# Kernel optimization log

Measured on AMD Instinct MI355X. Metric: run time of the kernel, lower is better.

## Reference

```python
import jax, jax.numpy as jnp
import numpy as np
from math import comb

G, NPG, D = 32, 128, 128   # graphs, nodes-per-graph, hidden dim
N = G * NPG                # 4096 nodes per side
E = 65536                  # edges per side (avg degree 16)
K = 6                      # Bernstein order (bern_k)
S, DCONV, DTR = 16, 4, 8   # mamba d_state, d_conv, dt_rank
HE = 27
SIGMAS = [1.0, 10.0, 100.0, 1000.0, 10000.0]


def _leaky(x, s=0.02):
    return jnp.where(x >= 0, x, s * x)


def _bnorm(x, g, b, eps=1e-5):
    m = jnp.mean(x, axis=0)
    v = jnp.var(x, axis=0)
    return (x - m) * jax.lax.rsqrt(v + eps) * g + b


def _bern_prop(x, src, dst, w, temp):
    # BernNet Bern_prop: Bernstein polynomial of sym-normalized Laplacian with weights relu(temp)
    n = x.shape[0]
    temp = jax.nn.relu(temp)
    deg = jax.ops.segment_sum(w, src, num_segments=n)
    dinv = jnp.where(deg > 0, 1.0 / jnp.sqrt(deg + 1e-12), 0.0)
    nw = (w * dinv[src] * dinv[dst])[:, None]
    adj = lambda v: jax.ops.segment_sum(nw * v[src], dst, num_segments=n)
    tmps = [x]
    xv = x
    for _ in range(K):
        xv = xv + adj(xv)          # (2I - L) v = v + A_norm v
        tmps.append(xv)
    out = (comb(K, 0) / 2 ** K) * temp[0] * tmps[K]
    for i in range(K):
        v = tmps[K - i - 1]
        for _ in range(i + 1):
            v = v - adj(v)         # L v = v - A_norm v
        out = out + (comb(K, i + 1) / 2 ** K) * temp[i + 1] * v
    return out


def _mamba(h, in_w, conv_w, conv_b, xproj_w, dt_w, dt_b, A_log, Dp, out_w):
    # Mamba block, d_model=D, expand=1 (d_inner=D), d_state=S, d_conv=DCONV
    Bb, L, _ = h.shape
    xq, z = jnp.split(h @ in_w, 2, axis=-1)             # [B,L,D] each
    xp = jnp.pad(xq, ((0, 0), (DCONV - 1, 0), (0, 0)))  # causal depthwise conv
    xc = conv_b + sum(xp[:, k:k + L, :] * conv_w[:, k] for k in range(DCONV))
    xc = jax.nn.silu(xc)
    dbl = xc @ xproj_w                                  # [B,L,DTR+2S]
    dt = jax.nn.softplus(dbl[..., :DTR] @ dt_w + dt_b)  # [B,L,D]
    Bm = dbl[..., DTR:DTR + S]
    Cm = dbl[..., DTR + S:]
    A = -jnp.exp(A_log)                                 # [D,S]
    dA = jnp.exp(dt[..., None] * A)                     # [B,L,D,S]
    dBx = dt[..., None] * Bm[:, :, None, :] * xc[..., None]

    def step(hs, ins):
        dA_t, dBx_t, C_t = ins
        hs = dA_t * hs + dBx_t
        return hs, jnp.einsum('bds,bs->bd', hs, C_t)

    h0 = jnp.zeros((Bb, D, S), h.dtype)
    _, ys = jax.lax.scan(step, h0, (jnp.swapaxes(dA, 0, 1),
                                    jnp.swapaxes(dBx, 0, 1),
                                    jnp.swapaxes(Cm, 0, 1)))
    y = jnp.swapaxes(ys, 0, 1) + xc * Dp
    return (y * jax.nn.silu(z)) @ out_w


def _xattn(q, k, v, mask):
    a = mask * (q @ k.T) - 1000.0 * (1.0 - mask)
    return jax.nn.softmax(a, axis=1) @ v


def setup_inputs():
    key = jax.random.key(0)
    ks = jax.random.split(key, 32)
    f = jnp.float32
    nrm = lambda k, shp, sc=1.0: jax.random.normal(k, shp, dtype=f) * sc
    h_lig = nrm(ks[0], (N, D), 0.5)
    h_rec = nrm(ks[1], (N, D), 0.5)
    x_lig = nrm(ks[2], (N, 3))
    x_rec = nrm(ks[3], (N, 3))
    he_1 = jax.random.uniform(ks[4], (E, HE), dtype=f)
    he_2 = jax.random.uniform(ks[5], (E, HE), dtype=f)
    g = (jnp.arange(E) // (E // G)).astype(jnp.int32)
    src1 = g * NPG + jax.random.randint(ks[6], (E,), 0, NPG, dtype=jnp.int32)
    dst1 = g * NPG + jax.random.randint(ks[7], (E,), 0, NPG, dtype=jnp.int32)
    src2 = g * NPG + jax.random.randint(ks[8], (E,), 0, NPG, dtype=jnp.int32)
    dst2 = g * NPG + jax.random.randint(ks[9], (E,), 0, NPG, dtype=jnp.int32)
    edge_index_1 = jnp.stack([src1, dst1])
    edge_index_2 = jnp.stack([src2, dst2])
    batch = (jnp.arange(N) // NPG).astype(jnp.int32)
    rng = np.random.default_rng(0)
    def mkperm(src):
        # lexsort([deg + noise, batch]) with batch as primary key
        deg = np.bincount(np.asarray(src), minlength=N).astype(np.float32)
        return jnp.asarray(np.lexsort((deg + rng.random(N).astype(np.float32),
                                       np.asarray(batch))).astype(np.int32))
    perm_1 = mkperm(src1)
    perm_2 = mkperm(src2)
    p = {}
    p['emlp_w1'] = nrm(ks[10], (32, D), 0.1)
    p['emlp_b1'] = jnp.zeros((D,), f)
    p['emlp_bn_g'] = jnp.ones((D,), f)
    p['emlp_bn_b'] = jnp.zeros((D,), f)
    p['emlp_w2'] = nrm(ks[11], (D, 1), 0.1)
    p['emlp_b2'] = jnp.zeros((1,), f)
    p['bern_temp'] = jnp.ones((K + 1,), f)
    p['m_in_w'] = nrm(ks[12], (D, 2 * D), 0.05)
    p['m_conv_w'] = nrm(ks[13], (D, DCONV), 0.2)
    p['m_conv_b'] = jnp.zeros((D,), f)
    p['m_xproj_w'] = nrm(ks[14], (D, DTR + 2 * S), 0.05)
    p['m_dt_w'] = nrm(ks[15], (DTR, D), 0.2)
    p['m_dt_b'] = jnp.full((D,), -4.0, f)
    p['m_A_log'] = jnp.log(jnp.broadcast_to(jnp.arange(1, S + 1, dtype=f), (D, S)))
    p['m_D'] = jnp.ones((D,), f)
    p['m_out_w'] = nrm(ks[16], (D, D), 0.05)
    p['q_w'] = nrm(ks[17], (D, D), 0.05)
    p['k_w'] = nrm(ks[18], (D, D), 0.05)
    p['v_w'] = nrm(ks[19], (D, D), 0.05)
    p['bn1_g'] = jnp.ones((D,), f)
    p['bn1_b'] = jnp.zeros((D,), f)
    p['bn2_g'] = jnp.ones((D,), f)
    p['bn2_b'] = jnp.zeros((D,), f)
    p['ff_w1'] = nrm(ks[20], (D, 2 * D), 0.05)
    p['ff_b1'] = jnp.zeros((2 * D,), f)
    p['ff_w2'] = nrm(ks[21], (2 * D, D), 0.05)
    p['ff_b2'] = jnp.zeros((D,), f)
    return dict(h_lig=h_lig, h_rec=h_rec, x_lig=x_lig, x_rec=x_rec,
                he_1=he_1, he_2=he_2, **p,
                edge_index_1=edge_index_1, edge_index_2=edge_index_2,
                batch_1=batch, batch_2=batch, perm_1=perm_1, perm_2=perm_2)


def reference(h_lig, h_rec, x_lig, x_rec, he_1, he_2,
              emlp_w1, emlp_b1, emlp_bn_g, emlp_bn_b, emlp_w2, emlp_b2,
              bern_temp, m_in_w, m_conv_w, m_conv_b, m_xproj_w, m_dt_w,
              m_dt_b, m_A_log, m_D, m_out_w, q_w, k_w, v_w,
              bn1_g, bn1_b, bn2_g, bn2_b, ff_w1, ff_b1, ff_w2, ff_b2,
              edge_index_1, edge_index_2, batch_1, batch_2, perm_1, perm_2):

    def side(h, x, he, ei, perm):
        src, dst = ei[0], ei[1]
        d2 = jnp.sum((x[src] - x[dst]) ** 2, axis=1, keepdims=True)
        ew = jnp.concatenate([jnp.exp(-d2 / s) for s in SIGMAS], axis=1)  # [E,5]
        t = _leaky(jnp.concatenate([ew, he], axis=1) @ emlp_w1 + emlp_b1)
        t = _bnorm(t, emlp_bn_g, emlp_bn_b)
        w = jax.nn.relu(t @ emlp_w2 + emlp_b2)[:, 0]                      # [E]
        h_local = _bern_prop(h, src, dst, w, bern_temp)
        inv = jnp.argsort(perm)
        hd = h[perm].reshape(G, NPG, D)   # uniform graph sizes -> exact dense batch
        ha = _mamba(hd, m_in_w, m_conv_w, m_conv_b, m_xproj_w, m_dt_w,
                    m_dt_b, m_A_log, m_D, m_out_w).reshape(N, D)[inv]
        return _bnorm(h + h_local + ha, bn1_g, bn1_b)

    hl = side(h_lig, x_lig, he_1, edge_index_1, perm_1)
    hr = side(h_rec, x_rec, he_2, edge_index_2, perm_2)
    mask = (batch_1[:, None] == batch_2[None, :]).astype(hl.dtype)
    cl = _xattn(_leaky(hl @ q_w), _leaky(hr @ k_w), hr @ v_w, mask)
    cr = _xattn(_leaky(hr @ q_w), _leaky(hl @ k_w), hl @ v_w, mask.T)
    hl = hl + cl
    hr = hr + cr
    ff = lambda h: jax.nn.relu(h @ ff_w1 + ff_b1) @ ff_w2 + ff_b2
    hl = _bnorm(hl + ff(hl), bn2_g, bn2_b)
    hr = _bnorm(hr + ff(hr), bn2_g, bn2_b)
    return hl, hr
```

## Files before the change

### kernel.cpp

```cpp
#include <hip/hip_runtime.h>
#include <math.h>

#define G_    32
#define NPG_  128
#define D_    128
#define N_    4096
#define E_    65536
#define ND_   (N_*D_)

#define W_OFF     0
#define DEG_OFF   65536
#define STATS_OFF 69632
#define BUF0      71680
#define HL_OFF    (BUF0 + 0*ND_)
#define HA_OFF    (BUF0 + 1*ND_)
#define X1_OFF    (BUF0 + 2*ND_)
#define HMID_OFF  (BUF0 + 3*ND_)
#define XC_OFF    (BUF0 + 4*ND_)
#define DTB_OFF   (BUF0 + 5*ND_)
#define YB_OFF    (BUF0 + 6*ND_)
#define XZ_OFF    (BUF0 + 7*ND_)
#define DBL_OFF   (BUF0 + 9*ND_)
#define SS_       ((size_t)(DBL_OFF + N_*40))

__device__ __forceinline__ float leakyf(float x){ return x >= 0.f ? x : 0.02f*x; }
__device__ __forceinline__ float siluf (float x){ return x / (1.f + expf(-x)); }

__device__ __forceinline__ void edge_feat(const float* __restrict__ x,
                                          const float* __restrict__ he,
                                          const int* __restrict__ ei,
                                          int e, float* feat, int& sN, int& dN)
{
  sN = ei[e]; dN = ei[E_ + e];
  float dx = x[sN*3+0]-x[dN*3+0];
  float dy = x[sN*3+1]-x[dN*3+1];
  float dz = x[sN*3+2]-x[dN*3+2];
  float d2 = dx*dx + dy*dy + dz*dz;
  feat[0] = expf(-d2/1.f);
  feat[1] = expf(-d2/10.f);
  feat[2] = expf(-d2/100.f);
  feat[3] = expf(-d2/1000.f);
  feat[4] = expf(-d2/10000.f);
#pragma unroll
  for (int j = 0; j < 27; ++j) feat[5+j] = he[(size_t)e*27 + j];
}

__global__ __launch_bounds__(256)
void edge_stats_kernel(const float* __restrict__ xl, const float* __restrict__ xr,
                       const float* __restrict__ hel, const float* __restrict__ her,
                       const int* __restrict__ ei1, const int* __restrict__ ei2,
                       const float* __restrict__ w1, const float* __restrict__ b1,
                       float* __restrict__ ws)
{
  int side = blockIdx.y;
  const float* x  = side ? xr  : xl;
  const float* he = side ? her : hel;
  const int*   ei = side ? ei2 : ei1;
  float* stats = ws + (size_t)side*SS_ + STATS_OFF;
  __shared__ float featl[256*36];
  __shared__ float csum[2][128], cssq[2][128];
  int tid = threadIdx.x;
  {
    int sN, dN; float feat[32];
    edge_feat(x, he, ei, blockIdx.x*256 + tid, feat, sN, dN);
#pragma unroll
    for (int j4 = 0; j4 < 8; ++j4)
      *(float4*)&featl[tid*36 + j4*4] = *(float4*)&feat[j4*4];
  }
  int c = tid & 127, hh = tid >> 7;
  float w1c[32];
#pragma unroll
  for (int j = 0; j < 32; ++j) w1c[j] = w1[j*128 + c];
  float b1c = b1[c];
  __syncthreads();
  float s1 = 0.f, s2 = 0.f;
  for (int e = 0; e < 128; ++e) {
    const float* f = &featl[(hh*128 + e)*36];
    float acc = b1c;
#pragma unroll
    for (int j4 = 0; j4 < 8; ++j4) {
      float4 f4 = *(const float4*)&f[j4*4];
      acc += f4.x*w1c[j4*4] + f4.y*w1c[j4*4+1] + f4.z*w1c[j4*4+2] + f4.w*w1c[j4*4+3];
    }
    float t = leakyf(acc);
    s1 += t; s2 += t*t;
  }
  csum[hh][c] = s1; cssq[hh][c] = s2;
  __syncthreads();
  if (tid < 128) {
    atomicAdd(&stats[tid],     csum[0][tid] + csum[1][tid]);
    atomicAdd(&stats[128+tid], cssq[0][tid] + cssq[1][tid]);
  }
}

__global__ void edge_finalize_kernel(const float* __restrict__ g_, const float* __restrict__ b_,
                                     const float* __restrict__ w2, const float* __restrict__ b2,
                                     float* __restrict__ ws)
{
  int side = blockIdx.y;
  float* stats = ws + (size_t)side*SS_ + STATS_OFF;
  __shared__ float red[128];
  int c = threadIdx.x;
  const float invE = 1.f/(float)E_;
  float mean = stats[c]*invE;
  float var  = fmaxf(stats[128+c]*invE - mean*mean, 0.f);
  float scale = rsqrtf(var + 1e-5f) * g_[c];
  stats[256+c] = scale * w2[c];
  red[c] = (b_[c] - mean*scale) * w2[c];
  __syncthreads();
  for (int off = 64; off; off >>= 1) { if (c < off) red[c] += red[c+off]; __syncthreads(); }
  if (c == 0) stats[384] = red[0] + b2[0];
}

__global__ __launch_bounds__(256)
void edge_w_kernel(const float* __restrict__ xl, const float* __restrict__ xr,
                   const float* __restrict__ hel, const float* __restrict__ her,
                   const int* __restrict__ ei1, const int* __restrict__ ei2,
                   const float* __restrict__ w1, const float* __restrict__ b1,
                   float* __restrict__ ws)
{
  int side = blockIdx.y;
  const float* x  = side ? xr  : xl;
  const float* he = side ? her : hel;
  const int*   ei = side ? ei2 : ei1;
  float* base = ws + (size_t)side*SS_;
  const float* stats = base + STATS_OFF;
  float* wbuf = base + W_OFF;
  float* deg  = base + DEG_OFF;
  __shared__ float w1t[128*32];
  __shared__ float b1l[128], all_[128];
  int tid = threadIdx.x;
  for (int i = tid; i < 4096; i += 256) {
    int j = i & 31, c = i >> 5;
    w1t[c*32 + j] = w1[j*128 + c];
  }
  if (tid < 128) { b1l[tid] = b1[tid]; all_[tid] = stats[256+tid]; }
  __syncthreads();
  int e = blockIdx.x*256 + tid;
  int sN, dN; float feat[32];
  edge_feat(x, he, ei, e, feat, sN, dN);
  float accw = stats[384];
  for (int c = 0; c < 128; ++c) {
    float acc = b1l[c];
#pragma unroll
    for (int j4 = 0; j4 < 8; ++j4) {
      float4 w4 = *(const float4*)&w1t[c*32 + j4*4];
      acc += feat[j4*4]*w4.x + feat[j4*4+1]*w4.y + feat[j4*4+2]*w4.z + feat[j4*4+3]*w4.w;
    }
    accw += leakyf(acc)*all_[c];
  }
  float w = fmaxf(accw, 0.f);
  wbuf[e] = w;
  atomicAdd(&deg[sN], w);
}

__global__ __launch_bounds__(256)
void bern_horner_kernel(const float* __restrict__ hl_in, const float* __restrict__ hr_in,
                        const int* __restrict__ ei1, const int* __restrict__ ei2,
                        const float* __restrict__ bern_temp, float* __restrict__ ws)
{
  int side = blockIdx.y;
  int g  = blockIdx.x >> 2;
  int d0 = (blockIdx.x & 3) * 32;
  const float* h  = side ? hr_in : hl_in;
  const int*   ei = side ? ei2 : ei1;
  float* base = ws + (size_t)side*SS_;
  const float* wbuf = base + W_OFF;
  const float* deg  = base + DEG_OFF;
  float* hloc = base + HL_OFF;

  __shared__ float A[128*132];
  __shared__ float v[128*32];
  int tid = threadIdx.x;
  for (int i = tid; i < 128*132; i += 256) A[i] = 0.f;

  const float btab[7][7] = {
    { 1,  6, 15,  20, 15,  6,  1},
    { 1,  4,  5,   0, -5, -4, -1},
    { 1,  2, -1,  -4, -1,  2,  1},
    { 1,  0, -3,   0,  3,  0, -1},
    { 1, -2, -1,   4, -1, -2,  1},
    { 1, -4,  5,   0, -5,  4, -1},
    { 1, -6, 15, -20, 15, -6,  1}};
  const float comb6[7] = {1,6,15,20,15,6,1};
  float a[7];
#pragma unroll
  for (int m = 0; m < 7; ++m) a[m] = 0.f;
#pragma unroll
  for (int j = 0; j < 7; ++j) {
    float tj = fmaxf(bern_temp[j], 0.f) * comb6[j] * (1.f/64.f);
#pragma unroll
    for (int m = 0; m < 7; ++m) a[m] += tj * btab[j][m];
  }
  __syncthreads();

  int ebase = g*2048, nbase = g*128;
  for (int i = tid; i < 2048; i += 256) {
    int e = ebase + i;
    int sN = ei[e], dN = ei[E_ + e];
    float ds_ = deg[sN], dd_ = deg[dN];
    float aa = ds_ > 0.f ? rsqrtf(ds_ + 1e-12f) : 0.f;
    float bb = dd_ > 0.f ? rsqrtf(dd_ + 1e-12f) : 0.f;
    atomicAdd(&A[(dN - nbase)*132 + (sN - nbase)], wbuf[e]*aa*bb);
  }

  const int db = (tid & 7)*4;
  const int rb = (tid >> 3)*4;
  float hreg[4][4], r[4][4], t[4][4];
#pragma unroll
  for (int i = 0; i < 4; ++i) {
    float4 h4 = *(const float4*)&h[(size_t)(nbase + rb + i)*128 + d0 + db];
    hreg[i][0]=h4.x; hreg[i][1]=h4.y; hreg[i][2]=h4.z; hreg[i][3]=h4.w;
#pragma unroll
    for (int jj = 0; jj < 4; ++jj) r[i][jj] = a[6]*hreg[i][jj];
  }

  for (int step = 5; step >= 0; --step) {
    __syncthreads();
#pragma unroll
    for (int i = 0; i < 4; ++i)
      *(float4*)&v[(rb+i)*32 + db] = make_float4(r[i][0], r[i][1], r[i][2], r[i][3]);
    __syncthreads();
#pragma unroll
    for (int i = 0; i < 4; ++i)
#pragma unroll
      for (int jj = 0; jj < 4; ++jj) t[i][jj] = 0.f;
    for (int k = 0; k < 128; k += 4) {
      float4 V0 = *(const float4*)&v[(k+0)*32 + db];
      float4 V1 = *(const float4*)&v[(k+1)*32 + db];
      float4 V2 = *(const float4*)&v[(k+2)*32 + db];
      float4 V3 = *(const float4*)&v[(k+3)*32 + db];
#pragma unroll
      for (int i = 0; i < 4; ++i) {
        float4 A4 = *(const float4*)&A[(rb+i)*132 + k];
        t[i][0] += A4.x*V0.x + A4.y*V1.x + A4.z*V2.x + A4.w*V3.x;
        t[i][1] += A4.x*V0.y + A4.y*V1.y + A4.z*V2.y + A4.w*V3.y;
        t[i][2] += A4.x*V0.z + A4.y*V1.z + A4.z*V2.z + A4.w*V3.z;
        t[i][3] += A4.x*V0.w + A4.y*V1.w + A4.z*V2.w + A4.w*V3.w;
      }
    }
    float ak = a[step];
#pragma unroll
    for (int i = 0; i < 4; ++i)
#pragma unroll
      for (int jj = 0; jj < 4; ++jj) r[i][jj] = t[i][jj] + ak*hreg[i][jj];
  }

#pragma unroll
  for (int i = 0; i < 4; ++i)
    *(float4*)&hloc[(size_t)(nbase + rb + i)*128 + d0 + db] =
        make_float4(r[i][0], r[i][1], r[i][2], r[i][3]);
}

template<int K, int NC, int TC, int CSPLIT, int ACT, int GATHER, int SCATTER, int ADDC, int BIAS>
__global__ __launch_bounds__(256)
void gemm_kernel(const float* __restrict__ A0, const float* __restrict__ A1, int lda,
                 const float* __restrict__ W, const float* __restrict__ bias,
                 float* __restrict__ C0, float* __restrict__ C1, int ldc,
                 const int* __restrict__ idx0, const int* __restrict__ idx1,
                 const float* __restrict__ add0, const float* __restrict__ add1)
{
  int side = blockIdx.y;
  const float* A = side ? A1 : A0;
  float* C = side ? C1 : C0;
  const int* idx = side ? idx1 : idx0;
  const float* addsrc = side ? add1 : add0;
  constexpr int RPT = TC/8;
  constexpr int CLEN = NC/CSPLIT;
  __shared__ float Alds[32][K];
  __shared__ float Wlds[K][TC];
  const int tid = threadIdx.x;
  const int r0 = (blockIdx.x / CSPLIT) * 32;
  const int cbase = (blockIdx.x % CSPLIT) * CLEN;
  for (int i = tid*4; i < 32*K; i += 1024) {
    int r = i / K, k = i % K;
    int row = GATHER ? idx[r0 + r] : (r0 + r);
    *(float4*)&Alds[r][k] = *(const float4*)&A[(size_t)row*lda + k];
  }
  for (int c0 = cbase; c0 < cbase + CLEN; c0 += TC) {
    __syncthreads();
    for (int i = tid*4; i < K*TC; i += 1024) {
      int k = i / TC, c = i % TC;
      if (c0 + c < NC) *(float4*)&Wlds[k][c] = *(const float4*)&W[k*NC + c0 + c];
      else             *(float4*)&Wlds[k][c] = make_float4(0.f,0.f,0.f,0.f);
    }
    __syncthreads();
    const int cl = tid % TC;
    const int rsub = (tid / TC) * RPT;
    float accv[RPT];
#pragma unroll
    for (int j = 0; j < RPT; ++j) accv[j] = 0.f;
    for (int k = 0; k < K; k += 4) {
      float w0 = Wlds[k][cl], w1v = Wlds[k+1][cl], w2v = Wlds[k+2][cl], w3v = Wlds[k+3][cl];
#pragma unroll
      for (int j = 0; j < RPT; ++j) {
        float4 a4 = *(const float4*)&Alds[rsub+j][k];
        accv[j] += a4.x*w0 + a4.y*w1v + a4.z*w2v + a4.w*w3v;
      }
    }
    int c = c0 + cl;
    if (c < NC) {
#pragma unroll
      for (int j = 0; j < RPT; ++j) {
        int row  = r0 + rsub + j;
        int orow = SCATTER ? idx[row] : row;
        float vv = accv[j];
        if (BIAS)     vv += bias[c];
        if (ACT == 1) vv = leakyf(vv);
        if (ACT == 2) vv = fmaxf(vv, 0.f);
        if (ADDC)     vv += addsrc[(size_t)orow*ldc + c];
        C[(size_t)orow*ldc + c] = vv;
      }
    }
  }
}

__global__ __launch_bounds__(256)
void qkv_kernel(const float* __restrict__ qw, const float* __restrict__ kw,
                const float* __restrict__ vw, float* __restrict__ ws)
{
  int side = blockIdx.y;
  int mat  = blockIdx.z;
  float* base = ws + (size_t)side*SS_;
  const float* A = base + HMID_OFF;
  const float* W = mat == 0 ? qw : (mat == 1 ? kw : vw);
  float* C = base + (mat == 0 ? XC_OFF : (mat == 1 ? DTB_OFF : YB_OFF));
  __shared__ float Alds[32][128];
  __shared__ float Wlds[128][64];
  const int tid = threadIdx.x;
  const int r0 = (blockIdx.x >> 1) * 32;
  const int c0 = (blockIdx.x & 1) * 64;
  for (int i = tid*4; i < 32*128; i += 1024)
    *(float4*)&Alds[i>>7][i&127] = *(const float4*)&A[(size_t)(r0 + (i>>7))*128 + (i&127)];
  for (int i = tid*4; i < 128*64; i += 1024)
    *(float4*)&Wlds[i>>6][i&63] = *(const float4*)&W[(i>>6)*128 + c0 + (i&63)];
  __syncthreads();
  const int cl = tid & 63;
  const int rsub = (tid >> 6) * 8;
  float accv[8];
#pragma unroll
  for (int j = 0; j < 8; ++j) accv[j] = 0.f;
  for (int k = 0; k < 128; k += 4) {
    float w0 = Wlds[k][cl], w1v = Wlds[k+1][cl], w2v = Wlds[k+2][cl], w3v = Wlds[k+3][cl];
#pragma unroll
    for (int j = 0; j < 8; ++j) {
      float4 a4 = *(const float4*)&Alds[rsub+j][k];
      accv[j] += a4.x*w0 + a4.y*w1v + a4.z*w2v + a4.w*w3v;
    }
  }
#pragma unroll
  for (int j = 0; j < 8; ++j) {
    float vv = accv[j];
    if (mat < 2) vv = leakyf(vv);
    C[(size_t)(r0 + rsub + j)*128 + c0 + cl] = vv;
  }
}

__global__ __launch_bounds__(256)
void conv_kernel(const float* __restrict__ cw, const float* __restrict__ cb, float* __restrict__ ws)
{
  int side = blockIdx.y;
  float* base = ws + (size_t)side*SS_;
  const float* xz = base + XZ_OFF;
  float* xc = base + XC_OFF;
  int i = blockIdx.x*256 + threadIdx.x;
  int j = i >> 7, d = i & 127;
  int l = j & 127;
  float a = cb[d];
#pragma unroll
  for (int k = 0; k < 4; ++k) {
    int ll = l - 3 + k;
    if (ll >= 0) a += xz[(size_t)(j-3+k)*256 + d] * cw[d*4 + k];
  }
  xc[i] = siluf(a);
}

__global__ __launch_bounds__(256)
void scan_kernel(const float* __restrict__ A_log, const float* __restrict__ Dp,
                 const float* __restrict__ dtw, const float* __restrict__ dtbias,
                 float* __restrict__ ws)
{
  int side = blockIdx.z;
  int g  = blockIdx.x;
  int d0 = blockIdx.y * 16;
  float* base = ws + (size_t)side*SS_;
  const float* dbl = base + DBL_OFF;
  const float* xcb = base + XC_OFF;
  float* xz = base + XZ_OFF;

  __shared__ float ldbl[128][40];
  __shared__ float lxc[128][16];
  __shared__ float ldt[128][16];
  __shared__ float lz[128][16];
  __shared__ float ly[128][16];
  __shared__ float ltw[8][16];
  __shared__ float ltb[16];

  int tid = threadIdx.x;
  int rowbase = g*128;
  if (tid < 128)      ltw[tid>>4][tid&15] = dtw[(tid>>4)*128 + d0 + (tid&15)];
  else if (tid < 144) ltb[tid-128] = dtbias[d0 + (tid-128)];
  for (int i = tid; i < 128*40; i += 256)
    ((float*)ldbl)[i] = dbl[(size_t)rowbase*40 + i];
  for (int i = tid; i < 2048; i += 256) {
    int l = i >> 4, dd = i & 15;
    lxc[l][dd] = xcb[(size_t)(rowbase+l)*128 + d0 + dd];
    lz[l][dd]  = xz[(size_t)(rowbase+l)*256 + 128 + d0 + dd];
  }
  __syncthreads();
  for (int i = tid; i < 2048; i += 256) {
    int l = i >> 4, dd = i & 15;
    float a = ltb[dd];
#pragma unroll
    for (int k = 0; k < 8; ++k) a += ldbl[l][k]*ltw[k][dd];
    ldt[l][dd] = a > 20.f ? a : log1pf(expf(a));
  }
  __syncthreads();

  int s = tid & 15, dl = (tid >> 4) & 15;
  float Ac  = -expf(A_log[(d0+dl)*16 + s]);
  float dpv = Dp[d0+dl];
  float hsv = 0.f;
  for (int l = 0; l < 128; ++l) {
    float dtv = ldt[l][dl];
    float xcv = lxc[l][dl];
    float Bv  = ldbl[l][8+s];
    float Cv  = ldbl[l][24+s];
    hsv = expf(dtv*Ac)*hsv + (dtv*xcv)*Bv;
    float val = hsv*Cv;
    val += __shfl_xor(val, 1, 16);
    val += __shfl_xor(val, 2, 16);
    val += __shfl_xor(val, 4, 16);
    val += __shfl_xor(val, 8, 16);
    if (s == 0) ly[l][dl] = val + xcv*dpv;
  }
  __syncthreads();
  for (int i = tid; i < 2048; i += 256) {
    int l = i >> 4, dd = i & 15;
    float y = ly[l][dd];
    float z = lz[l][dd];
    xz[(size_t)(rowbase+l)*256 + d0 + dd] = y * siluf(z);
  }
}

__global__ __launch_bounds__(256)
void stats_kernel(const float* __restrict__ hl_in, const float* __restrict__ hr_in,
                  float* __restrict__ ws, int mode, int statsoff)
{
  int side = blockIdx.y;
  float* base = ws + (size_t)side*SS_;
  const float* h    = side ? hr_in : hl_in;
  const float* hloc = base + HL_OFF;
  const float* ha   = base + HA_OFF;
  float* x1 = base + X1_OFF;
  float* stats = base + STATS_OFF + statsoff;
  int tid = threadIdx.x;
  int c = tid & 127;
  float s1 = 0.f, s2 = 0.f;
  for (int it = 0; it < 16; ++it) {
    int r = blockIdx.x*32 + (tid >> 7) + it*2;
    size_t i = (size_t)r*128 + c;
    float v;
    if (mode == 0) { v = h[i] + hloc[i] + ha[i]; x1[i] = v; }
    else           { v = ha[i]; }
    s1 += v; s2 += v*v;
  }
  __shared__ float red[256];
  red[tid] = s1; __syncthreads();
  if (tid < 128) atomicAdd(&stats[tid], red[tid] + red[tid+128]);
  __syncthreads();
  red[tid] = s2; __syncthreads();
  if (tid < 128) atomicAdd(&stats[128+tid], red[tid] + red[tid+128]);
}

__global__ void bn_finalize_kernel(const float* __restrict__ g_, const float* __restrict__ b_,
                                   float* __restrict__ ws, int statsoff, float invM)
{
  int side = blockIdx.y;
  float* stats = ws + (size_t)side*SS_ + STATS_OFF + statsoff;
  int c = threadIdx.x;
  float mean = stats[c]*invM;
  float var  = fmaxf(stats[128+c]*invM - mean*mean, 0.f);
  float scale = rsqrtf(var + 1e-5f) * g_[c];
  stats[256+c] = scale;
  stats[384+c] = b_[c] - mean*scale;
}

__global__ __launch_bounds__(256)
void bn_apply_kernel(float* __restrict__ ws, float* __restrict__ dout,
                     int srcoff, int dstoff, int statsoff, int to_dout)
{
  int side = blockIdx.y;
  float* base = ws + (size_t)side*SS_;
  const float* src = base + srcoff;
  const float* stats = base + STATS_OFF + statsoff;
  float* dst = to_dout ? (dout + (size_t)side*ND_) : (base + dstoff);
  size_t i = (size_t)blockIdx.x*256 + threadIdx.x;
  int c = (int)(i & 127);
  dst[i] = src[i]*stats[256+c] + stats[384+c];
}

__global__ __launch_bounds__(256)
void attn_kernel(float* __restrict__ ws)
{
  int dir = blockIdx.z;
  int g   = blockIdx.x;
  int rt  = blockIdx.y;
  float* baseq = ws + (size_t)dir*SS_;
  float* basek = ws + (size_t)(1-dir)*SS_;
  const float* qb = baseq + XC_OFF;
  const float* kb = basek + DTB_OFF;
  const float* vb = basek + YB_OFF;
  const float* hm = baseq + HMID_OFF;
  float* h2 = baseq + X1_OFF;
  __shared__ float kT[128*129];
  __shared__ float sp[32*128];
  int tid = threadIdx.x;
  for (int i = tid; i < 16384; i += 256) {
    int n = i >> 7, d = i & 127;
    kT[d*129 + n] = kb[(size_t)(g*128+n)*128 + d];
  }
  __syncthreads();
  int wv = tid >> 6, lane = tid & 63;
  for (int rl = wv; rl < 32; rl += 4) {
    int r = g*128 + rt*32 + rl;
    const float* qrow = qb + (size_t)r*128;
    float a0 = 0.f, a1 = 0.f;
    for (int d = 0; d < 128; ++d) {
      float qv = qrow[d];
      a0 += qv * kT[d*129 + lane];
      a1 += qv * kT[d*129 + 64 + lane];
    }
    float m = fmaxf(a0, a1);
#pragma unroll
    for (int off = 32; off; off >>= 1) m = fmaxf(m, __shfl_xor(m, off));
    float p0 = expf(a0 - m), p1 = expf(a1 - m);
    float ssum = p0 + p1;
#pragma unroll
    for (int off = 32; off; off >>= 1) ssum += __shfl_xor(ssum, off);
    float inv = 1.f/ssum;
    sp[rl*128 + lane]      = p0*inv;
    sp[rl*128 + 64 + lane] = p1*inv;
  }
  __syncthreads();
  for (int i = tid; i < 16384; i += 256) {
    int n = i >> 7, d = i & 127;
    kT[n*129 + d] = vb[(size_t)(g*128+n)*128 + d];
  }
  __syncthreads();
  for (int rl = wv; rl < 32; rl += 4) {
    int r = g*128 + rt*32 + rl;
    float a0 = 0.f, a1 = 0.f;
    const float* prow = sp + rl*128;
    for (int c = 0; c < 128; ++c) {
      float p = prow[c];
      a0 += p * kT[c*129 + lane];
      a1 += p * kT[c*129 + 64 + lane];
    }
    size_t o = (size_t)r*128;
    h2[o + lane]      = hm[o + lane]      + a0;
    h2[o + 64 + lane] = hm[o + 64 + lane] + a1;
  }
}

extern "C" void kernel_launch(void* const* d_in, const int* in_sizes, int n_in,
                              void* d_out, int out_size, void* d_ws, size_t ws_size,
                              hipStream_t stream)
{
  const float* h_lig     = (const float*)d_in[0];
  const float* h_rec     = (const float*)d_in[1];
  const float* x_lig     = (const float*)d_in[2];
  const float* x_rec     = (const float*)d_in[3];
  const float* he_1      = (const float*)d_in[4];
  const float* he_2      = (const float*)d_in[5];
  const float* emlp_w1   = (const float*)d_in[6];
  const float* emlp_b1   = (const float*)d_in[7];
  const float* emlp_bn_g = (const float*)d_in[8];
  const float* emlp_bn_b = (const float*)d_in[9];
  const float* emlp_w2   = (const float*)d_in[10];
  const float* emlp_b2   = (const float*)d_in[11];
  const float* bern_temp = (const float*)d_in[12];
  const float* m_in_w    = (const float*)d_in[13];
  const float* m_conv_w  = (const float*)d_in[14];
  const float* m_conv_b  = (const float*)d_in[15];
  const float* m_xproj_w = (const float*)d_in[16];
  const float* m_dt_w    = (const float*)d_in[17];
  const float* m_dt_b    = (const float*)d_in[18];
  const float* m_A_log   = (const float*)d_in[19];
  const float* m_D       = (const float*)d_in[20];
  const float* m_out_w   = (const float*)d_in[21];
  const float* q_w       = (const float*)d_in[22];
  const float* k_w       = (const float*)d_in[23];
  const float* v_w       = (const float*)d_in[24];
  const float* bn1_g     = (const float*)d_in[25];
  const float* bn1_b     = (const float*)d_in[26];
  const float* bn2_g     = (const float*)d_in[27];
  const float* bn2_b     = (const float*)d_in[28];
  const float* ff_w1     = (const float*)d_in[29];
  const float* ff_b1     = (const float*)d_in[30];
  const float* ff_w2     = (const float*)d_in[31];
  const float* ff_b2     = (const float*)d_in[32];
  const int*   ei1       = (const int*)d_in[33];
  const int*   ei2       = (const int*)d_in[34];
  const int*   perm1     = (const int*)d_in[37];
  const int*   perm2     = (const int*)d_in[38];

  float* ws   = (float*)d_ws;
  float* dout = (float*)d_out;

#define B0(off) (ws + (size_t)(off))
#define B1(off) (ws + SS_ + (size_t)(off))

  for (int s = 0; s < 2; ++s)
    hipMemsetAsync((char*)d_ws + ((size_t)s*SS_ + DEG_OFF)*sizeof(float), 0,
                   (N_ + 2048)*sizeof(float), stream);

  edge_stats_kernel<<<dim3(256,2), 256, 0, stream>>>(x_lig,x_rec,he_1,he_2,ei1,ei2,emlp_w1,emlp_b1,ws);
  edge_finalize_kernel<<<dim3(1,2), 128, 0, stream>>>(emlp_bn_g,emlp_bn_b,emlp_w2,emlp_b2,ws);
  edge_w_kernel<<<dim3(256,2), 256, 0, stream>>>(x_lig,x_rec,he_1,he_2,ei1,ei2,emlp_w1,emlp_b1,ws);

  bern_horner_kernel<<<dim3(G_*4,2), 256, 0, stream>>>(h_lig,h_rec,ei1,ei2,bern_temp,ws);

  gemm_kernel<128,256,64,4,0,1,0,0,0><<<dim3(512,2),256,0,stream>>>(
      h_lig,h_rec,128, m_in_w,nullptr, B0(XZ_OFF),B1(XZ_OFF),256, perm1,perm2, nullptr,nullptr);
  conv_kernel<<<dim3(2048,2), 256, 0, stream>>>(m_conv_w,m_conv_b,ws);
  gemm_kernel<128,40,64,1,0,0,0,0,0><<<dim3(128,2),256,0,stream>>>(
      B0(XC_OFF),B1(XC_OFF),128, m_xproj_w,nullptr, B0(DBL_OFF),B1(DBL_OFF),40, nullptr,nullptr, nullptr,nullptr);
  scan_kernel<<<dim3(32,8,2), 256, 0, stream>>>(m_A_log,m_D,m_dt_w,m_dt_b,ws);
  gemm_kernel<128,128,64,2,0,0,1,0,0><<<dim3(256,2),256,0,stream>>>(
      B0(XZ_OFF),B1(XZ_OFF),256, m_out_w,nullptr, B0(HA_OFF),B1(HA_OFF),128, perm1,perm2, nullptr,nullptr);

  stats_kernel<<<dim3(128,2), 256, 0, stream>>>(h_lig,h_rec,ws,0,512);
  bn_finalize_kernel<<<dim3(1,2), 128, 0, stream>>>(bn1_g,bn1_b,ws,512,1.f/(float)N_);
  bn_apply_kernel<<<dim3(2048,2), 256, 0, stream>>>(ws,dout,X1_OFF,HMID_OFF,512,0);

  qkv_kernel<<<dim3(256,2,3), 256, 0, stream>>>(q_w,k_w,v_w,ws);
  attn_kernel<<<dim3(32,4,2), 256, 0, stream>>>(ws);

  gemm_kernel<128,256,64,4,2,0,0,0,1><<<dim3(512,2),256,0,stream>>>(
      B0(X1_OFF),B1(X1_OFF),128, ff_w1,ff_b1, B0(XZ_OFF),B1(XZ_OFF),256, nullptr,nullptr, nullptr,nullptr);
  gemm_kernel<256,128,32,4,0,0,0,1,1><<<dim3(512,2),256,0,stream>>>(
      B0(XZ_OFF),B1(XZ_OFF),256, ff_w2,ff_b2, B0(HA_OFF),B1(HA_OFF),128, nullptr,nullptr, B0(X1_OFF),B1(X1_OFF));
  stats_kernel<<<dim3(128,2), 256, 0, stream>>>(h_lig,h_rec,ws,1,1024);
  bn_finalize_kernel<<<dim3(1,2), 128, 0, stream>>>(bn2_g,bn2_b,ws,1024,1.f/(float)N_);
  bn_apply_kernel<<<dim3(2048,2), 256, 0, stream>>>(ws,dout,HA_OFF,0,1024,1);
}
```

Measured before the change: 482.1 us.

## Materialize edge MLP hidden in bf16, fuse BN into attention, tile attention

The edge MLP hidden layer is now computed once with a register-tiled kernel and stored as bf16, reusing a large workspace region. Separate passes then reduce its batch-norm statistics and form the per-edge weights with a wave-level dot product. Before, the 32x128 product was recomputed in two passes. The first batch norm is folded into the QKV load and the attention epilogue, and the second into the output kernel, which removes the finalize and apply launches. Attention is rewritten as 4x4 register-tiled products from shared memory. Storing the hidden layer in bf16 adds rounding error to the edge weights and their statistics.

```diff
diff --git a/kernel.cpp b/kernel.cpp
--- a/kernel.cpp
+++ b/kernel.cpp
@@ -15,23 +15,30 @@
 #define HL_OFF    (BUF0 + 0*ND_)
 #define HA_OFF    (BUF0 + 1*ND_)
 #define X1_OFF    (BUF0 + 2*ND_)
-#define HMID_OFF  (BUF0 + 3*ND_)
-#define XC_OFF    (BUF0 + 4*ND_)
-#define DTB_OFF   (BUF0 + 5*ND_)
-#define YB_OFF    (BUF0 + 6*ND_)
-#define XZ_OFF    (BUF0 + 7*ND_)
-#define DBL_OFF   (BUF0 + 9*ND_)
+#define XC_OFF    (BUF0 + 3*ND_)
+#define DTB_OFF   (BUF0 + 4*ND_)
+#define YB_OFF    (BUF0 + 5*ND_)
+#define XZ_OFF    (BUF0 + 6*ND_)
+#define DBL_OFF   (BUF0 + 8*ND_)
 #define SS_       ((size_t)(DBL_OFF + N_*40))
 
 __device__ __forceinline__ float leakyf(float x){ return x >= 0.f ? x : 0.02f*x; }
 __device__ __forceinline__ float siluf (float x){ return x / (1.f + expf(-x)); }
+__device__ __forceinline__ unsigned short f2bf(float f){
+  unsigned int u = __float_as_uint(f);
+  u += 0x7FFF + ((u>>16)&1);
+  return (unsigned short)(u>>16);
+}
+__device__ __forceinline__ float bf2f(unsigned short s){
+  return __uint_as_float(((unsigned int)s)<<16);
+}
 
 __device__ __forceinline__ void edge_feat(const float* __restrict__ x,
                                           const float* __restrict__ he,
                                           const int* __restrict__ ei,
-                                          int e, float* feat, int& sN, int& dN)
-{
-  sN = ei[e]; dN = ei[E_ + e];
+                                          int e, float* feat)
+{
+  int sN = ei[e], dN = ei[E_ + e];
   float dx = x[sN*3+0]-x[dN*3+0];
   float dy = x[sN*3+1]-x[dN*3+1];
   float dz = x[sN*3+2]-x[dN*3+2];
@@ -46,74 +53,7 @@
 }
 
 __global__ __launch_bounds__(256)
-void edge_stats_kernel(const float* __restrict__ xl, const float* __restrict__ xr,
-                       const float* __restrict__ hel, const float* __restrict__ her,
-                       const int* __restrict__ ei1, const int* __restrict__ ei2,
-                       const float* __restrict__ w1, const float* __restrict__ b1,
-                       float* __restrict__ ws)
-{
-  int side = blockIdx.y;
-  const float* x  = side ? xr  : xl;
-  const float* he = side ? her : hel;
-  const int*   ei = side ? ei2 : ei1;
-  float* stats = ws + (size_t)side*SS_ + STATS_OFF;
-  __shared__ float featl[256*36];
-  __shared__ float csum[2][128], cssq[2][128];
-  int tid = threadIdx.x;
-  {
-    int sN, dN; float feat[32];
-    edge_feat(x, he, ei, blockIdx.x*256 + tid, feat, sN, dN);
-#pragma unroll
-    for (int j4 = 0; j4 < 8; ++j4)
-      *(float4*)&featl[tid*36 + j4*4] = *(float4*)&feat[j4*4];
-  }
-  int c = tid & 127, hh = tid >> 7;
-  float w1c[32];
-#pragma unroll
-  for (int j = 0; j < 32; ++j) w1c[j] = w1[j*128 + c];
-  float b1c = b1[c];
-  __syncthreads();
-  float s1 = 0.f, s2 = 0.f;
-  for (int e = 0; e < 128; ++e) {
-    const float* f = &featl[(hh*128 + e)*36];
-    float acc = b1c;
-#pragma unroll
-    for (int j4 = 0; j4 < 8; ++j4) {
-      float4 f4 = *(const float4*)&f[j4*4];
-      acc += f4.x*w1c[j4*4] + f4.y*w1c[j4*4+1] + f4.z*w1c[j4*4+2] + f4.w*w1c[j4*4+3];
-    }
-    float t = leakyf(acc);
-    s1 += t; s2 += t*t;
-  }
-  csum[hh][c] = s1; cssq[hh][c] = s2;
-  __syncthreads();
-  if (tid < 128) {
-    atomicAdd(&stats[tid],     csum[0][tid] + csum[1][tid]);
-    atomicAdd(&stats[128+tid], cssq[0][tid] + cssq[1][tid]);
-  }
-}
-
-__global__ void edge_finalize_kernel(const float* __restrict__ g_, const float* __restrict__ b_,
-                                     const float* __restrict__ w2, const float* __restrict__ b2,
-                                     float* __restrict__ ws)
-{
-  int side = blockIdx.y;
-  float* stats = ws + (size_t)side*SS_ + STATS_OFF;
-  __shared__ float red[128];
-  int c = threadIdx.x;
-  const float invE = 1.f/(float)E_;
-  float mean = stats[c]*invE;
-  float var  = fmaxf(stats[128+c]*invE - mean*mean, 0.f);
-  float scale = rsqrtf(var + 1e-5f) * g_[c];
-  stats[256+c] = scale * w2[c];
-  red[c] = (b_[c] - mean*scale) * w2[c];
-  __syncthreads();
-  for (int off = 64; off; off >>= 1) { if (c < off) red[c] += red[c+off]; __syncthreads(); }
-  if (c == 0) stats[384] = red[0] + b2[0];
-}
-
-__global__ __launch_bounds__(256)
-void edge_w_kernel(const float* __restrict__ xl, const float* __restrict__ xr,
+void edge_t_kernel(const float* __restrict__ xl, const float* __restrict__ xr,
                    const float* __restrict__ hel, const float* __restrict__ her,
                    const int* __restrict__ ei1, const int* __restrict__ ei2,
                    const float* __restrict__ w1, const float* __restrict__ b1,
@@ -123,35 +63,128 @@
   const float* x  = side ? xr  : xl;
   const float* he = side ? her : hel;
   const int*   ei = side ? ei2 : ei1;
+  unsigned short* T = (unsigned short*)(ws + (size_t)side*SS_ + BUF0);
+  __shared__ float F[256*36];
+  __shared__ float W1T[128*36];
+  __shared__ float b1l[128];
+  int tid = threadIdx.x;
+  int eb = blockIdx.x*256;
+  {
+    float feat[32];
+    edge_feat(x, he, ei, eb + tid, feat);
+#pragma unroll
+    for (int j4 = 0; j4 < 8; ++j4)
+      *(float4*)&F[tid*36 + j4*4] = *(float4*)&feat[j4*4];
+  }
+  for (int i = tid; i < 4096; i += 256) {
+    int c = i >> 5, k = i & 31;
+    W1T[c*36 + k] = w1[k*128 + c];
+  }
+  if (tid < 128) b1l[tid] = b1[tid];
+  __syncthreads();
+  int rg = tid >> 3, cg = tid & 7;
+  int e0 = rg*8;
+  for (int cb = 0; cb < 4; ++cb) {
+    int c0 = cb*32 + cg*4;
+    float acc[8][4];
+#pragma unroll
+    for (int i = 0; i < 8; ++i)
+#pragma unroll
+      for (int j = 0; j < 4; ++j) acc[i][j] = 0.f;
+    for (int k = 0; k < 32; k += 4) {
+      float4 W4[4];
+#pragma unroll
+      for (int j = 0; j < 4; ++j) W4[j] = *(const float4*)&W1T[(c0+j)*36 + k];
+#pragma unroll
+      for (int i = 0; i < 8; ++i) {
+        float4 F4 = *(const float4*)&F[(e0+i)*36 + k];
+#pragma unroll
+        for (int j = 0; j < 4; ++j)
+          acc[i][j] += F4.x*W4[j].x + F4.y*W4[j].y + F4.z*W4[j].z + F4.w*W4[j].w;
+      }
+    }
+#pragma unroll
+    for (int i = 0; i < 8; ++i) {
+      ushort4 o;
+      o.x = f2bf(leakyf(acc[i][0] + b1l[c0+0]));
+      o.y = f2bf(leakyf(acc[i][1] + b1l[c0+1]));
+      o.z = f2bf(leakyf(acc[i][2] + b1l[c0+2]));
+      o.w = f2bf(leakyf(acc[i][3] + b1l[c0+3]));
+      *(ushort4*)&T[(size_t)(eb + e0 + i)*128 + c0] = o;
+    }
+  }
+}
+
+__global__ __launch_bounds__(256)
+void tstats_kernel(float* __restrict__ ws)
+{
+  int side = blockIdx.y;
   float* base = ws + (size_t)side*SS_;
+  const unsigned short* T = (const unsigned short*)(base + BUF0);
+  float* stats = base + STATS_OFF;
+  int tid = threadIdx.x;
+  int c = tid & 127;
+  int r0 = blockIdx.x*512 + (tid >> 7)*256;
+  float s1 = 0.f, s2 = 0.f;
+  for (int r = r0; r < r0 + 256; ++r) {
+    float t = bf2f(T[(size_t)r*128 + c]);
+    s1 += t; s2 += t*t;
+  }
+  __shared__ float red[256];
+  red[tid] = s1; __syncthreads();
+  if (tid < 128) atomicAdd(&stats[tid], red[tid] + red[tid+128]);
+  __syncthreads();
+  red[tid] = s2; __syncthreads();
+  if (tid < 128) atomicAdd(&stats[128+tid], red[tid] + red[tid+128]);
+}
+
+__global__ __launch_bounds__(256)
+void edge_w_kernel(const float* __restrict__ g_, const float* __restrict__ b_,
+                   const float* __restrict__ w2, const float* __restrict__ b2,
+                   const int* __restrict__ ei1, const int* __restrict__ ei2,
+                   float* __restrict__ ws)
+{
+  int side = blockIdx.y;
+  const int* ei = side ? ei2 : ei1;
+  float* base = ws + (size_t)side*SS_;
+  const unsigned short* T = (const unsigned short*)(base + BUF0);
   const float* stats = base + STATS_OFF;
   float* wbuf = base + W_OFF;
   float* deg  = base + DEG_OFF;
-  __shared__ float w1t[128*32];
-  __shared__ float b1l[128], all_[128];
+  __shared__ float alpha[128];
+  __shared__ float red[128];
+  __shared__ float betav;
   int tid = threadIdx.x;
-  for (int i = tid; i < 4096; i += 256) {
-    int j = i & 31, c = i >> 5;
-    w1t[c*32 + j] = w1[j*128 + c];
-  }
-  if (tid < 128) { b1l[tid] = b1[tid]; all_[tid] = stats[256+tid]; }
-  __syncthreads();
-  int e = blockIdx.x*256 + tid;
-  int sN, dN; float feat[32];
-  edge_feat(x, he, ei, e, feat, sN, dN);
-  float accw = stats[384];
-  for (int c = 0; c < 128; ++c) {
-    float acc = b1l[c];
-#pragma unroll
-    for (int j4 = 0; j4 < 8; ++j4) {
-      float4 w4 = *(const float4*)&w1t[c*32 + j4*4];
-      acc += feat[j4*4]*w4.x + feat[j4*4+1]*w4.y + feat[j4*4+2]*w4.z + feat[j4*4+3]*w4.w;
-    }
-    accw += leakyf(acc)*all_[c];
-  }
-  float w = fmaxf(accw, 0.f);
-  wbuf[e] = w;
-  atomicAdd(&deg[sN], w);
+  const float invE = 1.f/(float)E_;
+  if (tid < 128) {
+    float mean = stats[tid]*invE;
+    float var  = fmaxf(stats[128+tid]*invE - mean*mean, 0.f);
+    float scale = rsqrtf(var + 1e-5f) * g_[tid];
+    alpha[tid] = scale * w2[tid];
+    red[tid] = (b_[tid] - mean*scale) * w2[tid];
+  }
+  __syncthreads();
+  for (int off = 64; off; off >>= 1) {
+    if (tid < off && tid + off < 128) red[tid] += red[tid+off];
+    __syncthreads();
+  }
+  if (tid == 0) betav = red[0] + b2[0];
+  __syncthreads();
+  int wv = tid >> 6, lane = tid & 63;
+  float a0 = alpha[lane*2], a1 = alpha[lane*2+1];
+  float beta = betav;
+  int ebase = blockIdx.x*256 + wv*64;
+  for (int e = ebase; e < ebase + 64; ++e) {
+    ushort2 tv = *(const ushort2*)&T[(size_t)e*128 + lane*2];
+    float acc = bf2f(tv.x)*a0 + bf2f(tv.y)*a1;
+#pragma unroll
+    for (int off = 32; off; off >>= 1) acc += __shfl_xor(acc, off);
+    if (lane == 0) {
+      float w = fmaxf(acc + beta, 0.f);
+      wbuf[e] = w;
+      atomicAdd(&deg[ei[e]], w);
+    }
+  }
 }
 
 __global__ __launch_bounds__(256)
@@ -317,21 +350,41 @@
 
 __global__ __launch_bounds__(256)
 void qkv_kernel(const float* __restrict__ qw, const float* __restrict__ kw,
-                const float* __restrict__ vw, float* __restrict__ ws)
+                const float* __restrict__ vw,
+                const float* __restrict__ g_, const float* __restrict__ b_,
+                float* __restrict__ ws)
 {
   int side = blockIdx.y;
   int mat  = blockIdx.z;
   float* base = ws + (size_t)side*SS_;
-  const float* A = base + HMID_OFF;
+  const float* A = base + X1_OFF;
+  const float* stats = base + STATS_OFF + 512;
   const float* W = mat == 0 ? qw : (mat == 1 ? kw : vw);
   float* C = base + (mat == 0 ? XC_OFF : (mat == 1 ? DTB_OFF : YB_OFF));
   __shared__ float Alds[32][128];
   __shared__ float Wlds[128][64];
+  __shared__ float scl[128], shl[128];
   const int tid = threadIdx.x;
+  if (tid < 128) {
+    float mean = stats[tid]*(1.f/(float)N_);
+    float var  = fmaxf(stats[128+tid]*(1.f/(float)N_) - mean*mean, 0.f);
+    float scale = rsqrtf(var + 1e-5f) * g_[tid];
+    scl[tid] = scale;
+    shl[tid] = b_[tid] - mean*scale;
+  }
+  __syncthreads();
   const int r0 = (blockIdx.x >> 1) * 32;
   const int c0 = (blockIdx.x & 1) * 64;
-  for (int i = tid*4; i < 32*128; i += 1024)
-    *(float4*)&Alds[i>>7][i&127] = *(const float4*)&A[(size_t)(r0 + (i>>7))*128 + (i&127)];
+  for (int i = tid*4; i < 32*128; i += 1024) {
+    int r = i >> 7, k = i & 127;
+    float4 a4 = *(const float4*)&A[(size_t)(r0 + r)*128 + k];
+    float4 s4 = *(const float4*)&scl[k];
+    float4 h4 = *(const float4*)&shl[k];
+    Alds[r][k+0] = a4.x*s4.x + h4.x;
+    Alds[r][k+1] = a4.y*s4.y + h4.y;
+    Alds[r][k+2] = a4.z*s4.z + h4.z;
+    Alds[r][k+3] = a4.w*s4.w + h4.w;
+  }
   for (int i = tid*4; i < 128*64; i += 1024)
     *(float4*)&Wlds[i>>6][i&63] = *(const float4*)&W[(i>>6)*128 + c0 + (i&63)];
   __syncthreads();
@@ -437,9 +490,7 @@
   __syncthreads();
   for (int i = tid; i < 2048; i += 256) {
     int l = i >> 4, dd = i & 15;
-    float y = ly[l][dd];
-    float z = lz[l][dd];
-    xz[(size_t)(rowbase+l)*256 + d0 + dd] = y * siluf(z);
+    xz[(size_t)(rowbase+l)*256 + d0 + dd] = ly[l][dd] * siluf(lz[l][dd]);
   }
 }
 
@@ -473,35 +524,26 @@
   if (tid < 128) atomicAdd(&stats[128+tid], red[tid] + red[tid+128]);
 }
 
-__global__ void bn_finalize_kernel(const float* __restrict__ g_, const float* __restrict__ b_,
-                                   float* __restrict__ ws, int statsoff, float invM)
-{
-  int side = blockIdx.y;
-  float* stats = ws + (size_t)side*SS_ + STATS_OFF + statsoff;
-  int c = threadIdx.x;
-  float mean = stats[c]*invM;
-  float var  = fmaxf(stats[128+c]*invM - mean*mean, 0.f);
-  float scale = rsqrtf(var + 1e-5f) * g_[c];
-  stats[256+c] = scale;
-  stats[384+c] = b_[c] - mean*scale;
-}
-
-__global__ __launch_bounds__(256)
-void bn_apply_kernel(float* __restrict__ ws, float* __restrict__ dout,
-                     int srcoff, int dstoff, int statsoff, int to_dout)
+__global__ __launch_bounds__(256)
+void bn_out_kernel(const float* __restrict__ g_, const float* __restrict__ b_,
+                   float* __restrict__ ws, float* __restrict__ dout)
 {
   int side = blockIdx.y;
   float* base = ws + (size_t)side*SS_;
-  const float* src = base + srcoff;
-  const float* stats = base + STATS_OFF + statsoff;
-  float* dst = to_dout ? (dout + (size_t)side*ND_) : (base + dstoff);
+  const float* src = base + HA_OFF;
+  const float* stats = base + STATS_OFF + 1024;
   size_t i = (size_t)blockIdx.x*256 + threadIdx.x;
   int c = (int)(i & 127);
-  dst[i] = src[i]*stats[256+c] + stats[384+c];
-}
-
-__global__ __launch_bounds__(256)
-void attn_kernel(float* __restrict__ ws)
+  float mean = stats[c]*(1.f/(float)N_);
+  float var  = fmaxf(stats[128+c]*(1.f/(float)N_) - mean*mean, 0.f);
+  float scale = rsqrtf(var + 1e-5f) * g_[c];
+  float shift = b_[c] - mean*scale;
+  dout[(size_t)side*ND_ + i] = src[i]*scale + shift;
+}
+
+__global__ __launch_bounds__(256)
+void attn_kernel(const float* __restrict__ g_, const float* __restrict__ b_,
+                 float* __restrict__ ws)
 {
   int dir = blockIdx.z;
   int g   = blockIdx.x;
@@ -511,55 +553,97 @@
   const float* qb = baseq + XC_OFF;
   const float* kb = basek + DTB_OFF;
   const float* vb = basek + YB_OFF;
-  const float* hm = baseq + HMID_OFF;
-  float* h2 = baseq + X1_OFF;
-  __shared__ float kT[128*129];
-  __shared__ float sp[32*128];
+  const float* stats = baseq + STATS_OFF + 512;
+  float* x1 = baseq + X1_OFF;
+  __shared__ float Kl[128*132];
+  __shared__ float Ql[32*132];
+  __shared__ float Pl[32*132];
+  __shared__ float scl[128], shl[128];
   int tid = threadIdx.x;
-  for (int i = tid; i < 16384; i += 256) {
-    int n = i >> 7, d = i & 127;
-    kT[d*129 + n] = kb[(size_t)(g*128+n)*128 + d];
-  }
-  __syncthreads();
-  int wv = tid >> 6, lane = tid & 63;
-  for (int rl = wv; rl < 32; rl += 4) {
-    int r = g*128 + rt*32 + rl;
-    const float* qrow = qb + (size_t)r*128;
-    float a0 = 0.f, a1 = 0.f;
-    for (int d = 0; d < 128; ++d) {
-      float qv = qrow[d];
-      a0 += qv * kT[d*129 + lane];
-      a1 += qv * kT[d*129 + 64 + lane];
-    }
-    float m = fmaxf(a0, a1);
-#pragma unroll
-    for (int off = 32; off; off >>= 1) m = fmaxf(m, __shfl_xor(m, off));
-    float p0 = expf(a0 - m), p1 = expf(a1 - m);
-    float ssum = p0 + p1;
-#pragma unroll
-    for (int off = 32; off; off >>= 1) ssum += __shfl_xor(ssum, off);
+  if (tid < 128) {
+    float mean = stats[tid]*(1.f/(float)N_);
+    float var  = fmaxf(stats[128+tid]*(1.f/(float)N_) - mean*mean, 0.f);
+    float scale = rsqrtf(var + 1e-5f) * g_[tid];
+    scl[tid] = scale;
+    shl[tid] = b_[tid] - mean*scale;
+  }
+  int rowg = g*128 + rt*32;
+  for (int i = tid*4; i < 32*128; i += 1024) {
+    int r = i >> 7, c = i & 127;
+    *(float4*)&Ql[r*132 + c] = *(const float4*)&qb[(size_t)(rowg + r)*128 + c];
+  }
+  for (int i = tid*4; i < 128*128; i += 1024) {
+    int r = i >> 7, c = i & 127;
+    *(float4*)&Kl[r*132 + c] = *(const float4*)&kb[(size_t)(g*128 + r)*128 + c];
+  }
+  __syncthreads();
+  int cg = tid & 31, rg = tid >> 5;
+  int r0l = rg*4, c0l = cg*4;
+  float S[4][4];
+#pragma unroll
+  for (int i = 0; i < 4; ++i)
+#pragma unroll
+    for (int j = 0; j < 4; ++j) S[i][j] = 0.f;
+  for (int k = 0; k < 128; k += 4) {
+    float4 K4[4];
+#pragma unroll
+    for (int j = 0; j < 4; ++j) K4[j] = *(const float4*)&Kl[(c0l+j)*132 + k];
+#pragma unroll
+    for (int i = 0; i < 4; ++i) {
+      float4 Q4 = *(const float4*)&Ql[(r0l+i)*132 + k];
+#pragma unroll
+      for (int j = 0; j < 4; ++j)
+        S[i][j] += Q4.x*K4[j].x + Q4.y*K4[j].y + Q4.z*K4[j].z + Q4.w*K4[j].w;
+    }
+  }
+#pragma unroll
+  for (int i = 0; i < 4; ++i) {
+    float m = fmaxf(fmaxf(S[i][0], S[i][1]), fmaxf(S[i][2], S[i][3]));
+#pragma unroll
+    for (int off = 16; off; off >>= 1) m = fmaxf(m, __shfl_xor(m, off));
+    float p0 = expf(S[i][0]-m), p1 = expf(S[i][1]-m), p2 = expf(S[i][2]-m), p3 = expf(S[i][3]-m);
+    float ssum = p0+p1+p2+p3;
+#pragma unroll
+    for (int off = 16; off; off >>= 1) ssum += __shfl_xor(ssum, off);
     float inv = 1.f/ssum;
-    sp[rl*128 + lane]      = p0*inv;
-    sp[rl*128 + 64 + lane] = p1*inv;
-  }
-  __syncthreads();
-  for (int i = tid; i < 16384; i += 256) {
-    int n = i >> 7, d = i & 127;
-    kT[n*129 + d] = vb[(size_t)(g*128+n)*128 + d];
-  }
-  __syncthreads();
-  for (int rl = wv; rl < 32; rl += 4) {
-    int r = g*128 + rt*32 + rl;
-    float a0 = 0.f, a1 = 0.f;
-    const float* prow = sp + rl*128;
-    for (int c = 0; c < 128; ++c) {
-      float p = prow[c];
-      a0 += p * kT[c*129 + lane];
-      a1 += p * kT[c*129 + 64 + lane];
-    }
-    size_t o = (size_t)r*128;
-    h2[o + lane]      = hm[o + lane]      + a0;
-    h2[o + 64 + lane] = hm[o + 64 + lane] + a1;
+    *(float4*)&Pl[(r0l+i)*132 + c0l] = make_float4(p0*inv, p1*inv, p2*inv, p3*inv);
+  }
+  __syncthreads();
+  for (int i = tid*4; i < 128*128; i += 1024) {
+    int r = i >> 7, c = i & 127;
+    *(float4*)&Kl[r*132 + c] = *(const float4*)&vb[(size_t)(g*128 + r)*128 + c];
+  }
+  __syncthreads();
+  float O[4][4];
+#pragma unroll
+  for (int i = 0; i < 4; ++i)
+#pragma unroll
+    for (int j = 0; j < 4; ++j) O[i][j] = 0.f;
+  for (int k = 0; k < 128; k += 4) {
+    float4 V0 = *(const float4*)&Kl[(k+0)*132 + c0l];
+    float4 V1 = *(const float4*)&Kl[(k+1)*132 + c0l];
+    float4 V2 = *(const float4*)&Kl[(k+2)*132 + c0l];
+    float4 V3 = *(const float4*)&Kl[(k+3)*132 + c0l];
+#pragma unroll
+    for (int i = 0; i < 4; ++i) {
+      float4 P4 = *(const float4*)&Pl[(r0l+i)*132 + k];
+      O[i][0] += P4.x*V0.x + P4.y*V1.x + P4.z*V2.x + P4.w*V3.x;
+      O[i][1] += P4.x*V0.y + P4.y*V1.y + P4.z*V2.y + P4.w*V3.y;
+      O[i][2] += P4.x*V0.z + P4.y*V1.z + P4.z*V2.z + P4.w*V3.z;
+      O[i][3] += P4.x*V0.w + P4.y*V1.w + P4.z*V2.w + P4.w*V3.w;
+    }
+  }
+  float4 s4 = *(const float4*)&scl[c0l];
+  float4 h4 = *(const float4*)&shl[c0l];
+#pragma unroll
+  for (int i = 0; i < 4; ++i) {
+    size_t o = (size_t)(rowg + r0l + i)*128 + c0l;
+    float4 xv = *(const float4*)&x1[o];
+    xv.x = xv.x*s4.x + h4.x + O[i][0];
+    xv.y = xv.y*s4.y + h4.y + O[i][1];
+    xv.z = xv.z*s4.z + h4.z + O[i][2];
+    xv.w = xv.w*s4.w + h4.w + O[i][3];
+    *(float4*)&x1[o] = xv;
   }
 }
 
@@ -615,9 +699,9 @@
     hipMemsetAsync((char*)d_ws + ((size_t)s*SS_ + DEG_OFF)*sizeof(float), 0,
                    (N_ + 2048)*sizeof(float), stream);
 
-  edge_stats_kernel<<<dim3(256,2), 256, 0, stream>>>(x_lig,x_rec,he_1,he_2,ei1,ei2,emlp_w1,emlp_b1,ws);
-  edge_finalize_kernel<<<dim3(1,2), 128, 0, stream>>>(emlp_bn_g,emlp_bn_b,emlp_w2,emlp_b2,ws);
-  edge_w_kernel<<<dim3(256,2), 256, 0, stream>>>(x_lig,x_rec,he_1,he_2,ei1,ei2,emlp_w1,emlp_b1,ws);
+  edge_t_kernel<<<dim3(256,2), 256, 0, stream>>>(x_lig,x_rec,he_1,he_2,ei1,ei2,emlp_w1,emlp_b1,ws);
+  tstats_kernel<<<dim3(128,2), 256, 0, stream>>>(ws);
+  edge_w_kernel<<<dim3(256,2), 256, 0, stream>>>(emlp_bn_g,emlp_bn_b,emlp_w2,emlp_b2,ei1,ei2,ws);
 
   bern_horner_kernel<<<dim3(G_*4,2), 256, 0, stream>>>(h_lig,h_rec,ei1,ei2,bern_temp,ws);
 
@@ -631,17 +715,14 @@
       B0(XZ_OFF),B1(XZ_OFF),256, m_out_w,nullptr, B0(HA_OFF),B1(HA_OFF),128, perm1,perm2, nullptr,nullptr);
 
   stats_kernel<<<dim3(128,2), 256, 0, stream>>>(h_lig,h_rec,ws,0,512);
-  bn_finalize_kernel<<<dim3(1,2), 128, 0, stream>>>(bn1_g,bn1_b,ws,512,1.f/(float)N_);
-  bn_apply_kernel<<<dim3(2048,2), 256, 0, stream>>>(ws,dout,X1_OFF,HMID_OFF,512,0);
-
-  qkv_kernel<<<dim3(256,2,3), 256, 0, stream>>>(q_w,k_w,v_w,ws);
-  attn_kernel<<<dim3(32,4,2), 256, 0, stream>>>(ws);
+
+  qkv_kernel<<<dim3(256,2,3), 256, 0, stream>>>(q_w,k_w,v_w,bn1_g,bn1_b,ws);
+  attn_kernel<<<dim3(32,4,2), 256, 0, stream>>>(bn1_g,bn1_b,ws);
 
   gemm_kernel<128,256,64,4,2,0,0,0,1><<<dim3(512,2),256,0,stream>>>(
       B0(X1_OFF),B1(X1_OFF),128, ff_w1,ff_b1, B0(XZ_OFF),B1(XZ_OFF),256, nullptr,nullptr, nullptr,nullptr);
   gemm_kernel<256,128,32,4,0,0,0,1,1><<<dim3(512,2),256,0,stream>>>(
       B0(XZ_OFF),B1(XZ_OFF),256, ff_w2,ff_b2, B0(HA_OFF),B1(HA_OFF),128, nullptr,nullptr, B0(X1_OFF),B1(X1_OFF));
   stats_kernel<<<dim3(128,2), 256, 0, stream>>>(h_lig,h_rec,ws,1,1024);
-  bn_finalize_kernel<<<dim3(1,2), 128, 0, stream>>>(bn2_g,bn2_b,ws,1024,1.f/(float)N_);
-  bn_apply_kernel<<<dim3(2048,2), 256, 0, stream>>>(ws,dout,HA_OFF,0,1024,1);
-}
+  bn_out_kernel<<<dim3(2048,2), 256, 0, stream>>>(bn2_g,bn2_b,ws,dout);
+}
```

Result: slower. 531.3 us (+10.2%).
